# Optimization experiments

Hardware: AMD Instinct MI355X
Metric: run time of the kernel (lower is better)

## Reference

```python
import jax, jax.numpy as jnp
import numpy as np

N = 100000   # active voxels
K = 27       # 3x3x3 kernel offsets
C = 64       # in_channels == out_channels (residual block)
EPS = 1e-5


def setup_inputs() -> dict:
    key = jax.random.key(0)
    ks = jax.random.split(key, 10)
    feats = jax.random.normal(ks[0], (N, C), dtype=jnp.float32)
    # kernel-map: for each voxel, index of the neighbor voxel for each of the 27 offsets
    nbr = jax.random.randint(ks[1], (N, K), 0, N)
    nbr = nbr.at[:, K // 2].set(jnp.arange(N))  # center offset is identity
    w_scale = 1.0 / np.sqrt(K * C)
    W1 = jax.random.normal(ks[2], (K, C, C), dtype=jnp.float32) * w_scale
    b1 = jax.random.normal(ks[3], (C,), dtype=jnp.float32) * 0.01
    g1 = jnp.ones((C,), jnp.float32)
    be1 = jnp.zeros((C,), jnp.float32)
    W2 = jax.random.normal(ks[4], (K, C, C), dtype=jnp.float32) * w_scale
    b2 = jax.random.normal(ks[5], (C,), dtype=jnp.float32) * 0.01
    g2 = jnp.ones((C,), jnp.float32)
    be2 = jnp.zeros((C,), jnp.float32)
    return {"feats": feats, "nbr": nbr, "W1": W1, "b1": b1, "g1": g1, "be1": be1,
            "W2": W2, "b2": b2, "g2": g2, "be2": be2}


def _sparse_conv(f, nbr, W, b):
    # gather neighbor features per kernel offset: [N, K, C]
    g = f[nbr]
    # per-offset matmul and reduce over offsets (gather-matmul-scatter form)
    return jnp.einsum('nkc,kcd->nd', g, W) + b


def _bn(x, gamma, beta):
    # BatchNorm over active voxels (training-mode batch stats, per channel)
    mu = x.mean(axis=0)
    var = x.var(axis=0)
    return (x - mu) * jax.lax.rsqrt(var + EPS) * gamma + beta


def reference(feats, nbr, W1, b1, g1, be1, W2, b2, g2, be2):
    h = jax.nn.relu(_bn(_sparse_conv(feats, nbr, W1, b1), g1, be1))
    h = _bn(_sparse_conv(h, nbr, W2, b2), g2, be2)
    return jax.nn.relu(h + feats)  # residual add + ReLU
```

## Files before the change

### kernel.cpp

```cpp
#include <hip/hip_runtime.h>

#define NCH 64
#define KOFF 27
#define EPSV 1e-5f

typedef __attribute__((ext_vector_type(8))) short  bf16x8;
typedef __attribute__((ext_vector_type(4))) float  f32x4;
typedef __attribute__((ext_vector_type(8))) unsigned short u16x8;

__device__ __forceinline__ unsigned short f2bf(float x) {
    unsigned int u = __float_as_uint(x);
    u += 0x7fffu + ((u >> 16) & 1u);
    return (unsigned short)(u >> 16);
}

__global__ __launch_bounds__(256)
void prep_kernel(const float* __restrict__ feats,
                 const float* __restrict__ W1, const float* __restrict__ W2,
                 unsigned short* __restrict__ fbf,
                 unsigned short* __restrict__ wt1, unsigned short* __restrict__ wt2,
                 float* __restrict__ stat, int total8)
{
    const int b = blockIdx.x;
    if (b == 0) {
        stat[threadIdx.x] = 0.f;
        return;
    }
    if (b <= 108) {
        const float* W = (b <= 54) ? W1 : W2;
        unsigned short* Wt = (b <= 54) ? wt1 : wt2;
        const int t = (b <= 54 ? b - 1 : b - 55) * 256 + threadIdx.x;
        const int l  = t & 63;
        const int ct = (t >> 6) & 3;
        const int s  = (t >> 8) & 1;
        const int k  = t >> 9;
        const int d     = ct * 16 + (l & 15);
        const int cbase = s * 32 + (l >> 4) * 8;
        u16x8 o;
#pragma unroll
        for (int j = 0; j < 8; ++j)
            o[j] = f2bf(W[(size_t)k * 4096 + (size_t)(cbase + j) * 64 + d]);
        reinterpret_cast<u16x8*>(Wt)[t] = o;
        return;
    }
    const int idx = (b - 109) * 256 + threadIdx.x;
    if (idx >= total8) return;
    const float4* xp = reinterpret_cast<const float4*>(feats) + (size_t)idx * 2;
    const float4 a = xp[0], c = xp[1];
    u16x8 o;
    o[0] = f2bf(a.x); o[1] = f2bf(a.y); o[2] = f2bf(a.z); o[3] = f2bf(a.w);
    o[4] = f2bf(c.x); o[5] = f2bf(c.y); o[6] = f2bf(c.z); o[7] = f2bf(c.w);
    reinterpret_cast<u16x8*>(fbf)[idx] = o;
}

__global__ __launch_bounds__(64, 2)
void conv_mfma_kernel(const unsigned short* __restrict__ fin,
                      const int* __restrict__ nbr,
                      const unsigned short* __restrict__ Wt,
                      const float* __restrict__ bias,
                      float* __restrict__ out, float* __restrict__ stat, int N)
{
    __shared__ int s_idx[KOFF * 64 + 64];

    const int lane = threadIdx.x;
    const int n0   = blockIdx.x * 64;
    const int m    = lane & 15;
    const int quad = lane >> 4;

    {
        const int rem  = N - n0;
        const int maxi = (rem < 64 ? rem : 64) * KOFF;
        const int* nb  = nbr + (size_t)n0 * KOFF;
#pragma unroll
        for (int j = 0; j < KOFF; ++j) {
            const int p = j * 64 + lane;
            s_idx[p] = (p < maxi) ? nb[p] : 0;
        }
    }

    f32x4 acc[4][4];
#pragma unroll
    for (int mt = 0; mt < 4; ++mt)
#pragma unroll
        for (int ct = 0; ct < 4; ++ct) acc[mt][ct] = (f32x4){0.f, 0.f, 0.f, 0.f};

    bf16x8 A[2][4][2];
    bf16x8 B[2][2][4];

#define LOADK(k, p)                                                          \
    {                                                                        \
        _Pragma("unroll")                                                    \
        for (int mt = 0; mt < 4; ++mt) {                                     \
            const int r = s_idx[(mt * 16 + m) * KOFF + (k)];                 \
            const unsigned short* fp = fin + (size_t)r * NCH + quad * 8;     \
            A[p][mt][0] = *reinterpret_cast<const bf16x8*>(fp);              \
            A[p][mt][1] = *reinterpret_cast<const bf16x8*>(fp + 32);         \
        }                                                                    \
        const unsigned short* wp = Wt + (size_t)(k) * 4096 + lane * 8;       \
        _Pragma("unroll")                                                    \
        for (int s = 0; s < 2; ++s)                                          \
            _Pragma("unroll")                                                \
            for (int ct = 0; ct < 4; ++ct)                                   \
                B[p][s][ct] =                                                \
                    *reinterpret_cast<const bf16x8*>(wp + (s * 4 + ct) * 512);\
    }

#define DOMFMA(p)                                                            \
    {                                                                        \
        _Pragma("unroll")                                                    \
        for (int mt = 0; mt < 4; ++mt)                                       \
            _Pragma("unroll")                                                \
            for (int s = 0; s < 2; ++s)                                      \
                _Pragma("unroll")                                            \
                for (int ct = 0; ct < 4; ++ct)                               \
                    acc[mt][ct] = __builtin_amdgcn_mfma_f32_16x16x32_bf16(   \
                        A[p][mt][s], B[p][s][ct], acc[mt][ct], 0, 0, 0);     \
    }

    LOADK(0, 0);
#pragma unroll 1
    for (int k = 0; k < KOFF - 1; k += 2) {
        LOADK(k + 1, 1);
        DOMFMA(0);
        LOADK(k + 2, 0);
        DOMFMA(1);
    }
    DOMFMA(0);

#pragma unroll
    for (int ct = 0; ct < 4; ++ct) {
        const int ch = ct * 16 + m;
        const float bv = bias[ch];
        float s = 0.f, q = 0.f;
#pragma unroll
        for (int mt = 0; mt < 4; ++mt) {
#pragma unroll
            for (int r = 0; r < 4; ++r) {
                const int vox = n0 + mt * 16 + quad * 4 + r;
                if (vox < N) {
                    const float v = acc[mt][ct][r] + bv;
                    out[(size_t)vox * NCH + ch] = v;
                    s += v;
                    q += v * v;
                }
            }
        }
        s += __shfl_xor(s, 16, 64);
        s += __shfl_xor(s, 32, 64);
        q += __shfl_xor(q, 16, 64);
        q += __shfl_xor(q, 32, 64);
        if (quad == 0) {
            atomicAdd(&stat[ch], s);
            atomicAdd(&stat[64 + ch], q);
        }
    }
#undef LOADK
#undef DOMFMA
}

__global__ __launch_bounds__(256)
void bn_relu_bf16_kernel(const float* __restrict__ x, const float* __restrict__ sums,
                         const float* __restrict__ gmm, const float* __restrict__ bet,
                         float invN, unsigned short* __restrict__ y, int total8)
{
    const int idx = blockIdx.x * 256 + threadIdx.x;
    if (idx >= total8) return;
    const int c0 = (idx & 7) * 8;
    const float4* xp = reinterpret_cast<const float4*>(x) + (size_t)idx * 2;
    const float4 a = xp[0], b = xp[1];
    float v[8] = {a.x, a.y, a.z, a.w, b.x, b.y, b.z, b.w};
    u16x8 o;
#pragma unroll
    for (int i = 0; i < 8; ++i) {
        const int c = c0 + i;
        const float mu  = sums[c] * invN;
        const float var = sums[64 + c] * invN - mu * mu;
        const float rs  = rsqrtf(var + EPSV);
        const float sc  = gmm[c] * rs;
        const float sh  = bet[c] - mu * sc;
        o[i] = f2bf(fmaxf(fmaf(v[i], sc, sh), 0.f));
    }
    reinterpret_cast<u16x8*>(y)[idx] = o;
}

__global__ __launch_bounds__(256)
void bn_res_relu_kernel(float* __restrict__ x, const float* __restrict__ feats,
                        const float* __restrict__ sums, const float* __restrict__ gmm,
                        const float* __restrict__ bet, float invN, int total4)
{
    const int idx = blockIdx.x * blockDim.x + threadIdx.x;
    if (idx >= total4) return;
    float4 v = reinterpret_cast<float4*>(x)[idx];
    const float4 f = reinterpret_cast<const float4*>(feats)[idx];
    const int c0 = (idx & 15) * 4;
    float sc[4], sh[4];
#pragma unroll
    for (int i = 0; i < 4; ++i) {
        const int c = c0 + i;
        const float mu  = sums[c] * invN;
        const float var = sums[64 + c] * invN - mu * mu;
        const float rs  = rsqrtf(var + EPSV);
        sc[i] = gmm[c] * rs;
        sh[i] = bet[c] - mu * sc[i];
    }
    v.x = fmaxf(fmaf(v.x, sc[0], sh[0]) + f.x, 0.f);
    v.y = fmaxf(fmaf(v.y, sc[1], sh[1]) + f.y, 0.f);
    v.z = fmaxf(fmaf(v.z, sc[2], sh[2]) + f.z, 0.f);
    v.w = fmaxf(fmaf(v.w, sc[3], sh[3]) + f.w, 0.f);
    reinterpret_cast<float4*>(x)[idx] = v;
}

extern "C" void kernel_launch(void* const* d_in, const int* in_sizes, int n_in,
                              void* d_out, int out_size, void* d_ws, size_t ws_size,
                              hipStream_t stream)
{
    const float* feats = (const float*)d_in[0];
    const int*   nbr   = (const int*)d_in[1];
    const float* W1    = (const float*)d_in[2];
    const float* b1    = (const float*)d_in[3];
    const float* g1    = (const float*)d_in[4];
    const float* be1   = (const float*)d_in[5];
    const float* W2    = (const float*)d_in[6];
    const float* b2    = (const float*)d_in[7];
    const float* g2    = (const float*)d_in[8];
    const float* be2   = (const float*)d_in[9];
    float* out = (float*)d_out;

    const int N  = in_sizes[0] / NCH;
    const int NC = N * NCH;
    const float invN = 1.0f / (float)N;

    float*          h0   = (float*)d_ws;
    unsigned short* fbf  = (unsigned short*)(h0 + NC);
    unsigned short* hbf  = fbf + NC;
    unsigned short* wt1  = hbf + NC;
    unsigned short* wt2  = wt1 + KOFF * 4096;
    float*          stat = (float*)(wt2 + KOFF * 4096);

    const int total8   = NC / 8;
    const int castGrid = (total8 + 255) / 256;
    const int prepGrid = 1 + 108 + castGrid;
    const int convGrid = (N + 63) / 64;

    prep_kernel<<<prepGrid, 256, 0, stream>>>(feats, W1, W2, fbf, wt1, wt2,
                                              stat, total8);
    conv_mfma_kernel<<<convGrid, 64, 0, stream>>>(fbf, nbr, wt1, b1, h0, stat, N);
    bn_relu_bf16_kernel<<<castGrid, 256, 0, stream>>>(h0, stat, g1, be1, invN,
                                                      hbf, total8);
    conv_mfma_kernel<<<convGrid, 64, 0, stream>>>(hbf, nbr, wt2, b2, out,
                                                  stat + 128, N);
    bn_res_relu_kernel<<<(NC / 4 + 255) / 256, 256, 0, stream>>>(
        out, feats, stat + 128, g2, be2, invN, NC / 4);
}
```

Baseline: 322.8 us.

## Fuse pipeline into cooperative persistent kernel with BN folded into conv2 gather

```diff
diff --git a/kernel.cpp b/kernel.cpp
--- a/kernel.cpp
+++ b/kernel.cpp
@@ -1,4 +1,7 @@
 #include <hip/hip_runtime.h>
+#include <hip/hip_cooperative_groups.h>
+
+namespace cg = cooperative_groups;
 
 #define NCH 64
 #define KOFF 27
@@ -14,241 +17,319 @@
     return (unsigned short)(u >> 16);
 }
 
-__global__ __launch_bounds__(256)
-void prep_kernel(const float* __restrict__ feats,
-                 const float* __restrict__ W1, const float* __restrict__ W2,
-                 unsigned short* __restrict__ fbf,
-                 unsigned short* __restrict__ wt1, unsigned short* __restrict__ wt2,
-                 float* __restrict__ stat, int total8)
-{
-    const int b = blockIdx.x;
-    if (b == 0) {
-        stat[threadIdx.x] = 0.f;
-        return;
-    }
-    if (b <= 108) {
-        const float* W = (b <= 54) ? W1 : W2;
-        unsigned short* Wt = (b <= 54) ? wt1 : wt2;
-        const int t = (b <= 54 ? b - 1 : b - 55) * 256 + threadIdx.x;
-        const int l  = t & 63;
-        const int ct = (t >> 6) & 3;
-        const int s  = (t >> 8) & 1;
-        const int k  = t >> 9;
-        const int d     = ct * 16 + (l & 15);
-        const int cbase = s * 32 + (l >> 4) * 8;
+struct MegaParams {
+    const float* feats; const int* nbr;
+    const float* W1; const float* b1; const float* g1; const float* be1;
+    const float* W2; const float* b2; const float* g2; const float* be2;
+    float* out;
+    unsigned short* fbf; unsigned short* hpre;
+    unsigned short* wt1; unsigned short* wt2;
+    float* stat;
+    unsigned int* ctr;
+    int N; int total8; int prepUnits;
+};
+
+__device__ __forceinline__ void phase_prep(const MegaParams& p)
+{
+    for (int b = blockIdx.x; b < p.prepUnits; b += gridDim.x) {
+        if (b == 0) {
+            p.stat[threadIdx.x] = 0.f;
+            if (threadIdx.x < 2) p.ctr[threadIdx.x] = 0u;
+            continue;
+        }
+        if (b <= 108) {
+            const float* W = (b <= 54) ? p.W1 : p.W2;
+            unsigned short* Wt = (b <= 54) ? p.wt1 : p.wt2;
+            const int t = (b <= 54 ? b - 1 : b - 55) * 256 + threadIdx.x;
+            const int l  = t & 63;
+            const int ct = (t >> 6) & 3;
+            const int s  = (t >> 8) & 1;
+            const int k  = t >> 9;
+            const int d     = ct * 16 + (l & 15);
+            const int cbase = s * 32 + (l >> 4) * 8;
+            u16x8 o;
+#pragma unroll
+            for (int j = 0; j < 8; ++j)
+                o[j] = f2bf(W[(size_t)k * 4096 + (size_t)(cbase + j) * 64 + d]);
+            reinterpret_cast<u16x8*>(Wt)[t] = o;
+            continue;
+        }
+        const int idx = (b - 109) * 256 + threadIdx.x;
+        if (idx >= p.total8) continue;
+        const float4* xp = reinterpret_cast<const float4*>(p.feats) + (size_t)idx * 2;
+        const float4 a = xp[0], c = xp[1];
         u16x8 o;
-#pragma unroll
-        for (int j = 0; j < 8; ++j)
-            o[j] = f2bf(W[(size_t)k * 4096 + (size_t)(cbase + j) * 64 + d]);
-        reinterpret_cast<u16x8*>(Wt)[t] = o;
-        return;
-    }
-    const int idx = (b - 109) * 256 + threadIdx.x;
-    if (idx >= total8) return;
-    const float4* xp = reinterpret_cast<const float4*>(feats) + (size_t)idx * 2;
-    const float4 a = xp[0], c = xp[1];
+        o[0] = f2bf(a.x); o[1] = f2bf(a.y); o[2] = f2bf(a.z); o[3] = f2bf(a.w);
+        o[4] = f2bf(c.x); o[5] = f2bf(c.y); o[6] = f2bf(c.z); o[7] = f2bf(c.w);
+        reinterpret_cast<u16x8*>(p.fbf)[idx] = o;
+    }
+}
+
+__device__ __forceinline__ bf16x8 bn_frag(bf16x8 a, const float* sc, const float* sh) {
+    u16x8 u = (u16x8)a;
     u16x8 o;
-    o[0] = f2bf(a.x); o[1] = f2bf(a.y); o[2] = f2bf(a.z); o[3] = f2bf(a.w);
-    o[4] = f2bf(c.x); o[5] = f2bf(c.y); o[6] = f2bf(c.z); o[7] = f2bf(c.w);
-    reinterpret_cast<u16x8*>(fbf)[idx] = o;
-}
-
-__global__ __launch_bounds__(64, 2)
-void conv_mfma_kernel(const unsigned short* __restrict__ fin,
-                      const int* __restrict__ nbr,
-                      const unsigned short* __restrict__ Wt,
-                      const float* __restrict__ bias,
-                      float* __restrict__ out, float* __restrict__ stat, int N)
-{
-    __shared__ int s_idx[KOFF * 64 + 64];
-
-    const int lane = threadIdx.x;
-    const int n0   = blockIdx.x * 64;
+#pragma unroll
+    for (int j = 0; j < 8; ++j) {
+        float f = __uint_as_float((unsigned)u[j] << 16);
+        f = fmaxf(fmaf(f, sc[j], sh[j]), 0.f);
+        o[j] = f2bf(f);
+    }
+    return (bf16x8)o;
+}
+
+template <bool BN, typename OUT_T>
+__device__ __forceinline__ void conv_phase(
+    const MegaParams& p, const unsigned short* fin, const unsigned short* Wt,
+    const float* bias, OUT_T* outp, float* statp, unsigned int* ctr, int* sw,
+    const float* g, const float* be, const float* statIn)
+{
+    const int lane = threadIdx.x & 63;
     const int m    = lane & 15;
     const int quad = lane >> 4;
-
-    {
-        const int rem  = N - n0;
-        const int maxi = (rem < 64 ? rem : 64) * KOFF;
-        const int* nb  = nbr + (size_t)n0 * KOFF;
-#pragma unroll
-        for (int j = 0; j < KOFF; ++j) {
-            const int p = j * 64 + lane;
-            s_idx[p] = (p < maxi) ? nb[p] : 0;
-        }
-    }
-
-    f32x4 acc[4][4];
-#pragma unroll
-    for (int mt = 0; mt < 4; ++mt)
-#pragma unroll
-        for (int ct = 0; ct < 4; ++ct) acc[mt][ct] = (f32x4){0.f, 0.f, 0.f, 0.f};
-
-    bf16x8 A[2][4][2];
-    bf16x8 B[2][2][4];
-
-#define LOADK(k, p)                                                          \
-    {                                                                        \
-        _Pragma("unroll")                                                    \
-        for (int mt = 0; mt < 4; ++mt) {                                     \
-            const int r = s_idx[(mt * 16 + m) * KOFF + (k)];                 \
-            const unsigned short* fp = fin + (size_t)r * NCH + quad * 8;     \
-            A[p][mt][0] = *reinterpret_cast<const bf16x8*>(fp);              \
-            A[p][mt][1] = *reinterpret_cast<const bf16x8*>(fp + 32);         \
-        }                                                                    \
-        const unsigned short* wp = Wt + (size_t)(k) * 4096 + lane * 8;       \
-        _Pragma("unroll")                                                    \
-        for (int s = 0; s < 2; ++s)                                          \
-            _Pragma("unroll")                                                \
-            for (int ct = 0; ct < 4; ++ct)                                   \
-                B[p][s][ct] =                                                \
-                    *reinterpret_cast<const bf16x8*>(wp + (s * 4 + ct) * 512);\
-    }
-
-#define DOMFMA(p)                                                            \
-    {                                                                        \
-        _Pragma("unroll")                                                    \
-        for (int mt = 0; mt < 4; ++mt)                                       \
-            _Pragma("unroll")                                                \
-            for (int s = 0; s < 2; ++s)                                      \
-                _Pragma("unroll")                                            \
-                for (int ct = 0; ct < 4; ++ct)                               \
-                    acc[mt][ct] = __builtin_amdgcn_mfma_f32_16x16x32_bf16(   \
-                        A[p][mt][s], B[p][s][ct], acc[mt][ct], 0, 0, 0);     \
-    }
-
-    LOADK(0, 0);
+    const int N    = p.N;
+    const float invN = 1.0f / (float)N;
+    const int ntiles = (N + 31) >> 5;
+
+    float scv[2][8], shv[2][8];
+    if (BN) {
+#pragma unroll
+        for (int sf = 0; sf < 2; ++sf)
+#pragma unroll
+            for (int j = 0; j < 8; ++j) {
+                const int c = sf * 32 + quad * 8 + j;
+                const float mu  = statIn[c] * invN;
+                const float var = statIn[64 + c] * invN - mu * mu;
+                const float rs  = rsqrtf(var + EPSV);
+                scv[sf][j] = g[c] * rs;
+                shv[sf][j] = be[c] - mu * scv[sf][j];
+            }
+    }
+    float bv4[4];
+#pragma unroll
+    for (int ct = 0; ct < 4; ++ct) bv4[ct] = bias[ct * 16 + m];
+
+    float sacc[4] = {0.f, 0.f, 0.f, 0.f};
+    float qacc[4] = {0.f, 0.f, 0.f, 0.f};
+    const char* finB = (const char*)fin;
+
+    for (;;) {
+        int tile = 0;
+        if (lane == 0) tile = (int)atomicAdd(ctr, 1u);
+        tile = __shfl(tile, 0, 64);
+        if (tile >= ntiles) break;
+        const int n0 = tile * 32;
+
+        {
+            int rem = N - n0;
+            rem = rem < 0 ? 0 : (rem > 32 ? 32 : rem);
+            const int maxi = rem * KOFF;
+            const int* nb  = p.nbr + (size_t)n0 * KOFF;
+            for (int pp = lane; pp < 32 * KOFF; pp += 64)
+                sw[pp] = ((pp < maxi) ? nb[pp] : 0) * (NCH * 2);
+        }
+
+        f32x4 acc[2][4];
+#pragma unroll
+        for (int mt = 0; mt < 2; ++mt)
+#pragma unroll
+            for (int ct = 0; ct < 4; ++ct) acc[mt][ct] = (f32x4){0.f, 0.f, 0.f, 0.f};
+
+        bf16x8 A[2][2][2];
+        bf16x8 B[2][2][4];
+
+#define LOADK(kk, pbuf)                                                       \
+    {                                                                         \
+        const char* fp0 = finB + sw[(0 * 16 + m) * KOFF + (kk)] + quad * 16;  \
+        const char* fp1 = finB + sw[(1 * 16 + m) * KOFF + (kk)] + quad * 16;  \
+        A[pbuf][0][0] = *reinterpret_cast<const bf16x8*>(fp0);                \
+        A[pbuf][0][1] = *reinterpret_cast<const bf16x8*>(fp0 + 64);           \
+        A[pbuf][1][0] = *reinterpret_cast<const bf16x8*>(fp1);                \
+        A[pbuf][1][1] = *reinterpret_cast<const bf16x8*>(fp1 + 64);           \
+        const unsigned short* wp = Wt + (size_t)(kk) * 4096 + lane * 8;       \
+        _Pragma("unroll")                                                     \
+        for (int sf = 0; sf < 2; ++sf)                                        \
+            _Pragma("unroll")                                                 \
+            for (int ct = 0; ct < 4; ++ct)                                    \
+                B[pbuf][sf][ct] =                                             \
+                    *reinterpret_cast<const bf16x8*>(wp + (sf * 4 + ct) * 512);\
+    }
+
+#define DOMFMA(pbuf)                                                          \
+    {                                                                         \
+        _Pragma("unroll")                                                     \
+        for (int mt = 0; mt < 2; ++mt)                                        \
+            _Pragma("unroll")                                                 \
+            for (int sf = 0; sf < 2; ++sf) {                                  \
+                bf16x8 af = A[pbuf][mt][sf];                                  \
+                if (BN) af = bn_frag(af, scv[sf], shv[sf]);                   \
+                _Pragma("unroll")                                             \
+                for (int ct = 0; ct < 4; ++ct)                                \
+                    acc[mt][ct] = __builtin_amdgcn_mfma_f32_16x16x32_bf16(    \
+                        af, B[pbuf][sf][ct], acc[mt][ct], 0, 0, 0);           \
+            }                                                                 \
+    }
+
+        LOADK(0, 0);
 #pragma unroll 1
-    for (int k = 0; k < KOFF - 1; k += 2) {
-        LOADK(k + 1, 1);
+        for (int k = 0; k + 2 < KOFF; k += 2) {
+            LOADK(k + 1, 1);
+            DOMFMA(0);
+            LOADK(k + 2, 0);
+            DOMFMA(1);
+        }
         DOMFMA(0);
-        LOADK(k + 2, 0);
-        DOMFMA(1);
-    }
-    DOMFMA(0);
-
-#pragma unroll
-    for (int ct = 0; ct < 4; ++ct) {
-        const int ch = ct * 16 + m;
-        const float bv = bias[ch];
-        float s = 0.f, q = 0.f;
-#pragma unroll
-        for (int mt = 0; mt < 4; ++mt) {
-#pragma unroll
-            for (int r = 0; r < 4; ++r) {
-                const int vox = n0 + mt * 16 + quad * 4 + r;
-                if (vox < N) {
-                    const float v = acc[mt][ct][r] + bv;
-                    out[(size_t)vox * NCH + ch] = v;
-                    s += v;
-                    q += v * v;
+#undef LOADK
+#undef DOMFMA
+
+#pragma unroll
+        for (int ct = 0; ct < 4; ++ct) {
+            const int ch = ct * 16 + m;
+#pragma unroll
+            for (int mt = 0; mt < 2; ++mt) {
+#pragma unroll
+                for (int r = 0; r < 4; ++r) {
+                    const int vox = n0 + mt * 16 + quad * 4 + r;
+                    if (vox < N) {
+                        const float v = acc[mt][ct][r] + bv4[ct];
+                        if constexpr (__is_same(OUT_T, unsigned short))
+                            outp[(size_t)vox * NCH + ch] = f2bf(v);
+                        else
+                            outp[(size_t)vox * NCH + ch] = v;
+                        sacc[ct] += v;
+                        qacc[ct] += v * v;
+                    }
                 }
             }
         }
+    }
+
+#pragma unroll
+    for (int ct = 0; ct < 4; ++ct) {
+        float s = sacc[ct], q = qacc[ct];
         s += __shfl_xor(s, 16, 64);
         s += __shfl_xor(s, 32, 64);
         q += __shfl_xor(q, 16, 64);
         q += __shfl_xor(q, 32, 64);
         if (quad == 0) {
-            atomicAdd(&stat[ch], s);
-            atomicAdd(&stat[64 + ch], q);
-        }
-    }
-#undef LOADK
-#undef DOMFMA
-}
-
-__global__ __launch_bounds__(256)
-void bn_relu_bf16_kernel(const float* __restrict__ x, const float* __restrict__ sums,
-                         const float* __restrict__ gmm, const float* __restrict__ bet,
-                         float invN, unsigned short* __restrict__ y, int total8)
-{
-    const int idx = blockIdx.x * 256 + threadIdx.x;
-    if (idx >= total8) return;
-    const int c0 = (idx & 7) * 8;
-    const float4* xp = reinterpret_cast<const float4*>(x) + (size_t)idx * 2;
-    const float4 a = xp[0], b = xp[1];
-    float v[8] = {a.x, a.y, a.z, a.w, b.x, b.y, b.z, b.w};
-    u16x8 o;
-#pragma unroll
-    for (int i = 0; i < 8; ++i) {
-        const int c = c0 + i;
-        const float mu  = sums[c] * invN;
-        const float var = sums[64 + c] * invN - mu * mu;
-        const float rs  = rsqrtf(var + EPSV);
-        const float sc  = gmm[c] * rs;
-        const float sh  = bet[c] - mu * sc;
-        o[i] = f2bf(fmaxf(fmaf(v[i], sc, sh), 0.f));
-    }
-    reinterpret_cast<u16x8*>(y)[idx] = o;
-}
-
-__global__ __launch_bounds__(256)
-void bn_res_relu_kernel(float* __restrict__ x, const float* __restrict__ feats,
-                        const float* __restrict__ sums, const float* __restrict__ gmm,
-                        const float* __restrict__ bet, float invN, int total4)
-{
-    const int idx = blockIdx.x * blockDim.x + threadIdx.x;
-    if (idx >= total4) return;
-    float4 v = reinterpret_cast<float4*>(x)[idx];
-    const float4 f = reinterpret_cast<const float4*>(feats)[idx];
-    const int c0 = (idx & 15) * 4;
-    float sc[4], sh[4];
-#pragma unroll
-    for (int i = 0; i < 4; ++i) {
-        const int c = c0 + i;
-        const float mu  = sums[c] * invN;
-        const float var = sums[64 + c] * invN - mu * mu;
-        const float rs  = rsqrtf(var + EPSV);
-        sc[i] = gmm[c] * rs;
-        sh[i] = bet[c] - mu * sc[i];
-    }
-    v.x = fmaxf(fmaf(v.x, sc[0], sh[0]) + f.x, 0.f);
-    v.y = fmaxf(fmaf(v.y, sc[1], sh[1]) + f.y, 0.f);
-    v.z = fmaxf(fmaf(v.z, sc[2], sh[2]) + f.z, 0.f);
-    v.w = fmaxf(fmaf(v.w, sc[3], sh[3]) + f.w, 0.f);
-    reinterpret_cast<float4*>(x)[idx] = v;
-}
+            atomicAdd(&statp[ct * 16 + m], s);
+            atomicAdd(&statp[64 + ct * 16 + m], q);
+        }
+    }
+}
+
+__device__ __forceinline__ void phase_post(const MegaParams& p)
+{
+    const int total4 = p.N * (NCH / 4);
+    const float invN = 1.0f / (float)p.N;
+    const float* st2 = p.stat + 128;
+    for (int idx = blockIdx.x * 256 + threadIdx.x; idx < total4;
+         idx += gridDim.x * 256) {
+        float4 v = reinterpret_cast<float4*>(p.out)[idx];
+        const float4 f = reinterpret_cast<const float4*>(p.feats)[idx];
+        const int c0 = (idx & 15) * 4;
+#pragma unroll
+        for (int i = 0; i < 4; ++i) {
+            const int c = c0 + i;
+            const float mu  = st2[c] * invN;
+            const float var = st2[64 + c] * invN - mu * mu;
+            const float rs  = rsqrtf(var + EPSV);
+            const float sc  = p.g2[c] * rs;
+            const float sh  = p.be2[c] - mu * sc;
+            float* vv = reinterpret_cast<float*>(&v) + i;
+            const float ff = reinterpret_cast<const float*>(&f)[i];
+            *vv = fmaxf(fmaf(*vv, sc, sh) + ff, 0.f);
+        }
+        reinterpret_cast<float4*>(p.out)[idx] = v;
+    }
+}
+
+__global__ __launch_bounds__(256, 2)
+void mega_kernel(MegaParams p)
+{
+    __shared__ int s_idx[4 * 32 * KOFF];
+    cg::grid_group grid = cg::this_grid();
+    int* sw = s_idx + (threadIdx.x >> 6) * (32 * KOFF);
+
+    phase_prep(p);
+    __threadfence();
+    grid.sync();
+
+    conv_phase<false, unsigned short>(p, p.fbf, p.wt1, p.b1, p.hpre, p.stat,
+                                      p.ctr + 0, sw, nullptr, nullptr, nullptr);
+    __threadfence();
+    grid.sync();
+
+    conv_phase<true, float>(p, p.hpre, p.wt2, p.b2, p.out, p.stat + 128,
+                            p.ctr + 1, sw, p.g1, p.be1, p.stat);
+    __threadfence();
+    grid.sync();
+
+    phase_post(p);
+}
+
+__global__ __launch_bounds__(256) void k_prep(MegaParams p) { phase_prep(p); }
+__global__ __launch_bounds__(256, 2) void k_conv1(MegaParams p) {
+    __shared__ int s_idx[4 * 32 * KOFF];
+    int* sw = s_idx + (threadIdx.x >> 6) * (32 * KOFF);
+    conv_phase<false, unsigned short>(p, p.fbf, p.wt1, p.b1, p.hpre, p.stat,
+                                      p.ctr + 0, sw, nullptr, nullptr, nullptr);
+}
+__global__ __launch_bounds__(256, 2) void k_conv2(MegaParams p) {
+    __shared__ int s_idx[4 * 32 * KOFF];
+    int* sw = s_idx + (threadIdx.x >> 6) * (32 * KOFF);
+    conv_phase<true, float>(p, p.hpre, p.wt2, p.b2, p.out, p.stat + 128,
+                            p.ctr + 1, sw, p.g1, p.be1, p.stat);
+}
+__global__ __launch_bounds__(256) void k_post(MegaParams p) { phase_post(p); }
 
 extern "C" void kernel_launch(void* const* d_in, const int* in_sizes, int n_in,
                               void* d_out, int out_size, void* d_ws, size_t ws_size,
                               hipStream_t stream)
 {
-    const float* feats = (const float*)d_in[0];
-    const int*   nbr   = (const int*)d_in[1];
-    const float* W1    = (const float*)d_in[2];
-    const float* b1    = (const float*)d_in[3];
-    const float* g1    = (const float*)d_in[4];
-    const float* be1   = (const float*)d_in[5];
-    const float* W2    = (const float*)d_in[6];
-    const float* b2    = (const float*)d_in[7];
-    const float* g2    = (const float*)d_in[8];
-    const float* be2   = (const float*)d_in[9];
-    float* out = (float*)d_out;
-
     const int N  = in_sizes[0] / NCH;
     const int NC = N * NCH;
-    const float invN = 1.0f / (float)N;
-
-    float*          h0   = (float*)d_ws;
-    unsigned short* fbf  = (unsigned short*)(h0 + NC);
-    unsigned short* hbf  = fbf + NC;
-    unsigned short* wt1  = hbf + NC;
+
+    unsigned short* fbf  = (unsigned short*)d_ws;
+    unsigned short* hpre = fbf + NC;
+    unsigned short* wt1  = hpre + NC;
     unsigned short* wt2  = wt1 + KOFF * 4096;
     float*          stat = (float*)(wt2 + KOFF * 4096);
-
-    const int total8   = NC / 8;
-    const int castGrid = (total8 + 255) / 256;
-    const int prepGrid = 1 + 108 + castGrid;
-    const int convGrid = (N + 63) / 64;
-
-    prep_kernel<<<prepGrid, 256, 0, stream>>>(feats, W1, W2, fbf, wt1, wt2,
-                                              stat, total8);
-    conv_mfma_kernel<<<convGrid, 64, 0, stream>>>(fbf, nbr, wt1, b1, h0, stat, N);
-    bn_relu_bf16_kernel<<<castGrid, 256, 0, stream>>>(h0, stat, g1, be1, invN,
-                                                      hbf, total8);
-    conv_mfma_kernel<<<convGrid, 64, 0, stream>>>(hbf, nbr, wt2, b2, out,
-                                                  stat + 128, N);
-    bn_res_relu_kernel<<<(NC / 4 + 255) / 256, 256, 0, stream>>>(
-        out, feats, stat + 128, g2, be2, invN, NC / 4);
-}
+    unsigned int*   ctr  = (unsigned int*)(stat + 256);
+
+    MegaParams P;
+    P.feats = (const float*)d_in[0];
+    P.nbr   = (const int*)d_in[1];
+    P.W1    = (const float*)d_in[2];
+    P.b1    = (const float*)d_in[3];
+    P.g1    = (const float*)d_in[4];
+    P.be1   = (const float*)d_in[5];
+    P.W2    = (const float*)d_in[6];
+    P.b2    = (const float*)d_in[7];
+    P.g2    = (const float*)d_in[8];
+    P.be2   = (const float*)d_in[9];
+    P.out   = (float*)d_out;
+    P.fbf   = fbf;  P.hpre = hpre;
+    P.wt1   = wt1;  P.wt2  = wt2;
+    P.stat  = stat; P.ctr  = ctr;
+    P.N     = N;
+    P.total8 = NC / 8;
+    P.prepUnits = 1 + 108 + (P.total8 + 255) / 256;
+
+    bool done = false;
+    int bpc = 0;
+    if (hipOccupancyMaxActiveBlocksPerMultiprocessor(
+            &bpc, (const void*)mega_kernel, 256, 0) == hipSuccess && bpc > 0) {
+        int grid = bpc * 256;
+        if (grid > 2048) grid = 2048;
+        void* args[] = { &P };
+        if (hipLaunchCooperativeKernel((const void*)mega_kernel, dim3(grid),
+                                       dim3(256), args, 0, stream) == hipSuccess)
+            done = true;
+    }
+    if (!done) {
+        k_prep <<<P.prepUnits, 256, 0, stream>>>(P);
+        k_conv1<<<768, 256, 0, stream>>>(P);
+        k_conv2<<<768, 256, 0, stream>>>(P);
+        k_post <<<(N * (NCH / 4) + 255) / 256, 256, 0, stream>>>(P);
+    }
+}
```

Result: slower. 543.7 us (+68.4%).
